# Kernel tuning notes

Measured on AMD Instinct MI355X. Metric: run time of the kernel, lower is better.

## Reference

```python
import jax, jax.numpy as jnp
import numpy as np


def conv2d(x, w, pad=0, groups=1, bias=None):
    out = jax.lax.conv_general_dilated(
        x, w, (1, 1), [(pad, pad), (pad, pad)],
        dimension_numbers=('NCHW', 'OIHW', 'NCHW'), feature_group_count=groups)
    return out if bias is None else out + bias[None, :, None, None]


def l2norm(t):
    # F.normalize(t, dim=-1): divide by max(||t||_2, 1e-12)
    return t / jnp.maximum(jnp.sqrt(jnp.sum(t * t, axis=-1, keepdims=True)), 1e-12)


def chan_attn(q, k, v, temp, heads):
    # transposed (channel) attention: contract over N=H*W, softmax over small channel dim
    b, _, h, w = v.shape
    n = h * w
    q = l2norm(q.reshape(b, heads, -1, n))
    k = l2norm(k.reshape(b, heads, -1, n))
    v = v.reshape(b, heads, -1, n)
    attn = jax.nn.softmax(jnp.einsum('bhdn,bhen->bhde', q, k) * temp, axis=-1)
    return jnp.einsum('bhde,bhen->bhdn', attn, v).reshape(b, -1, h, w)


def nearest_resize(x, H, W):
    # torch F.interpolate(mode='nearest'): idx = floor(i * in/out)
    hi, wi = x.shape[2], x.shape[3]
    iy = jnp.arange(H) * hi // H
    ix = jnp.arange(W) * wi // W
    return x[:, :, iy][:, :, :, ix]


def deform_conv(x, offsets, w, bias, k, pad, groups):
    # torchvision DeformConv2d, stride=1, dilation=1, offset layout [B, 2*k*k, H, W] as (dy, dx) pairs
    B, Cin, H, W = x.shape
    K2 = k * k
    off = offsets.reshape(B, K2, 2, H, W)
    ky, kx = jnp.meshgrid(jnp.arange(k), jnp.arange(k), indexing='ij')
    py = (jnp.arange(H)[None, None, :, None] - pad) + ky.reshape(1, K2, 1, 1) + off[:, :, 0]
    px = (jnp.arange(W)[None, None, None, :] - pad) + kx.reshape(1, K2, 1, 1) + off[:, :, 1]
    y0f = jnp.floor(py); x0f = jnp.floor(px)
    wy = (py - y0f)[:, None]  # [B,1,K2,H,W]
    wx = (px - x0f)[:, None]
    y0 = y0f.astype(jnp.int32); x0 = x0f.astype(jnp.int32)
    xf = x.reshape(B, Cin, H * W)

    def gather(yi, xi):
        valid = ((yi >= 0) & (yi < H) & (xi >= 0) & (xi < W)).astype(x.dtype)
        idx = (jnp.clip(yi, 0, H - 1) * W + jnp.clip(xi, 0, W - 1)).reshape(B, 1, -1)
        v = jnp.take_along_axis(xf, idx, axis=2).reshape(B, Cin, K2, H, W)
        return v * valid[:, None]

    s = (gather(y0, x0) * (1 - wy) * (1 - wx)
         + gather(y0, x0 + 1) * (1 - wy) * wx
         + gather(y0 + 1, x0) * wy * (1 - wx)
         + gather(y0 + 1, x0 + 1) * wy * wx)  # [B, Cin, K2, H, W]
    g = groups
    s = s.reshape(B, g, Cin // g, K2, H, W)
    wg = w.reshape(g, w.shape[0] // g, Cin // g, K2)
    out = jnp.einsum('bgckhw,gock->bgohw', s, wg).reshape(B, -1, H, W)
    return out + bias[None, :, None, None]


def scconv(x, w_k2, w_k3, w_k4):
    B, C, H, W = x.shape
    p = x.reshape(B, C, H // 2, 2, W // 2, 2).mean(axis=(3, 5))  # AvgPool2d(2,2)
    a = jax.nn.sigmoid(nearest_resize(conv2d(p, w_k2, pad=0), H, W))
    return conv2d(conv2d(x, w_k3, pad=1) * a, w_k4, pad=1)


def layernorm_c(x, g, b):
    # LayerNorm over channel dim of NCHW (applied as [B, HW, C] in the original)
    b_, c, h, w = x.shape
    t = x.reshape(b_, c, h * w).transpose(0, 2, 1)
    mu = t.mean(-1, keepdims=True)
    var = ((t - mu) ** 2).mean(-1, keepdims=True)
    t = (t - mu) / jnp.sqrt(var + 1e-5) * g + b
    return t.transpose(0, 2, 1).reshape(b_, c, h, w)


def _forward(x, y, temp, w_po, w_lp1, w_lp2, ln_g, ln_b, temp_in, w_qkv, w_qkvd,
             w_mproj, w_c3, w_k2, w_k3, w_k4, w_d3, b_d3, w_d5, b_d5, w_d7, b_d7,
             w_pw, b_pw):
    b, c, h, w = x.shape
    heads = 8
    # --- Multi_Receptive_Attentive_Prompts ---
    l1 = conv2d(x, w_lp1)
    l2 = conv2d(x, w_lp2, pad=1)
    xn = layernorm_c(x, ln_g, ln_b)
    qkv = conv2d(conv2d(xn, w_qkv), w_qkvd, pad=1, groups=c)
    qi, ki, vi = jnp.split(qkv, 3, axis=1)
    xg = x + conv2d(chan_attn(qi, ki, vi, temp_in, heads), w_mproj)
    prompt = conv2d(jnp.concatenate([l1, l2, xg], axis=1), w_c3, pad=1)
    # --- Temporal_Alignment ---
    offs = scconv(jnp.concatenate([x, y], axis=1), w_k2, w_k3, w_k4)  # [B,166,H,W]
    f3 = jax.nn.relu(deform_conv(x, offs[:, :18], w_d3, b_d3, 3, 1, 8))
    f5 = jax.nn.relu(deform_conv(x, offs[:, 18:68], w_d5, b_d5, 5, 2, 8))
    f7 = jax.nn.relu(deform_conv(x, offs[:, 68:166], w_d7, b_d7, 7, 3, 8))
    k_feat = conv2d(jnp.concatenate([f3, f5, f7], axis=1), w_pw, bias=b_pw)
    # --- prompted channel attention ---
    q_feat = jnp.concatenate([x, prompt], axis=1)  # 2c channels -> d_q = 2c/heads
    out = chan_attn(q_feat, k_feat, x, temp, heads)  # [B, 2c, H, W]
    return conv2d(out, w_po)


def setup_inputs() -> dict:
    key = jax.random.key(0)
    ks = jax.random.split(key, 16)
    C, B, H, W = 32, 2, 128, 128
    r = lambda k, shp: jax.random.normal(k, shp, dtype=jnp.float32) * 0.05
    return {
        'x': jax.random.normal(ks[0], (B, C, H, W), dtype=jnp.float32),
        'y': jax.random.normal(ks[1], (B, C, H, W), dtype=jnp.float32),
        'temp': jnp.ones((1, 8, 1, 1), jnp.float32),
        'w_po': r(ks[2], (C, 2 * C, 1, 1)),
        'w_lp1': r(ks[3], (C, C, 1, 1)),
        'w_lp2': r(ks[4], (C, C, 3, 3)),
        'ln_g': jnp.ones((C,), jnp.float32),
        'ln_b': jnp.zeros((C,), jnp.float32),
        'temp_in': jnp.ones((1, 8, 1, 1), jnp.float32),
        'w_qkv': r(ks[5], (3 * C, C, 1, 1)),
        'w_qkvd': r(ks[6], (3 * C, 3, 3, 3)),  # groups=C: in/groups = 3
        'w_mproj': r(ks[7], (C, C, 1, 1)),
        'w_c3': r(ks[8], (C, 3 * C, 3, 3)),
        'w_k2': r(ks[9], (166, 2 * C, 3, 3)),
        'w_k3': r(ks[10], (166, 2 * C, 3, 3)),
        'w_k4': r(ks[11], (166, 166, 3, 3)),
        'w_d3': r(ks[12], (C, C // 8, 3, 3)),
        'b_d3': jnp.zeros((C,), jnp.float32),
        'w_d5': r(ks[13], (C, C // 8, 5, 5)),
        'b_d5': jnp.zeros((C,), jnp.float32),
        'w_d7': r(ks[14], (C, C // 8, 7, 7)),
        'b_d7': jnp.zeros((C,), jnp.float32),
        'w_pw': r(ks[15], (C, 3 * C, 1, 1)),
        'b_pw': jnp.zeros((C,), jnp.float32),
    }


def reference(x, y, temp, w_po, w_lp1, w_lp2, ln_g, ln_b, temp_in, w_qkv, w_qkvd,
              w_mproj, w_c3, w_k2, w_k3, w_k4, w_d3, b_d3, w_d5, b_d5, w_d7, b_d7,
              w_pw, b_pw):
    return _forward(x, y, temp, w_po, w_lp1, w_lp2, ln_g, ln_b, temp_in, w_qkv,
                    w_qkvd, w_mproj, w_c3, w_k2, w_k3, w_k4, w_d3, b_d3, w_d5,
                    b_d5, w_d7, b_d7, w_pw, b_pw)
```

## Files before the change

### kernel.cpp

```cpp
#include <hip/hip_runtime.h>
#include <hip/hip_bf16.h>
#include <hip/hip_fp16.h>


constexpr int B = 2, C = 32, H = 128, W = 128, N = H * W;

using bh8   = __attribute__((ext_vector_type(8))) short;
using f32x4 = __attribute__((ext_vector_type(4))) float;

__device__ __forceinline__ ushort f2bf(float v) {
  __hip_bfloat16 h = __float2bfloat16(v);
  return *(ushort*)&h;
}
__device__ __forceinline__ float bf2f(ushort u) {
  union { unsigned int i; float f; } w; w.i = ((unsigned int)u) << 16; return w.f;
}

__global__ __launch_bounds__(256) void k_prep(const float* __restrict__ x,
                                              const float* __restrict__ y,
                                              const float* __restrict__ ln_g,
                                              const float* __restrict__ ln_b,
                                              float* __restrict__ cat2,
                                              ushort* __restrict__ xtb,
                                              ushort* __restrict__ cat2b,
                                              float* __restrict__ xn,
                                              ushort* __restrict__ poolb) {
  __shared__ float tile[C][257];
  const int b = blockIdx.y, n0 = blockIdx.x * 256, tid = threadIdx.x;
  const int n = n0 + tid;
  const int prow = blockIdx.x;
  for (int c = 0; c < C; c++) {
    float v = x[(size_t)(b * C + c) * N + n];
    tile[c][tid] = v;
    cat2[(size_t)(b * 64 + c) * N + n] = v;
  }
  __syncthreads();
  {
    float s = 0.f, ss = 0.f;
#pragma unroll
    for (int c = 0; c < C; c++) { const float v = tile[c][tid]; s += v; ss += v * v; }
    const float mu = s * (1.f / C);
    const float var = ss * (1.f / C) - mu * mu;
    const float inv = rsqrtf(var + 1e-5f);
#pragma unroll
    for (int c = 0; c < C; c++)
      xn[(size_t)(b * C + c) * N + n] = (tile[c][tid] - mu) * inv * ln_g[c] + ln_b[c];
  }
  for (int i = tid; i < C * 256; i += 256) {
    int c = i & 31, nl = i >> 5;
    const ushort bv = f2bf(tile[c][nl]);
    xtb[((size_t)b * N + n0 + nl) * 32 + c] = bv;
    cat2b[((size_t)b * N + n0 + nl) * 64 + c] = bv;
  }
  for (int i = tid; i < 2048; i += 256) {
    const int ox = i >> 5, c = i & 31;
    const float pv = 0.25f * (tile[c][2 * ox] + tile[c][2 * ox + 1]
                            + tile[c][128 + 2 * ox] + tile[c][128 + 2 * ox + 1]);
    poolb[((size_t)b * 4096 + prow * 64 + ox) * 64 + c] = f2bf(pv);
  }
  __syncthreads();
  for (int c = 0; c < C; c++) {
    float v = y[(size_t)(b * C + c) * N + n];
    tile[c][tid] = v;
    cat2[(size_t)(b * 64 + 32 + c) * N + n] = v;
  }
  __syncthreads();
  for (int i = tid; i < C * 256; i += 256) {
    int c = i & 31, nl = i >> 5;
    cat2b[((size_t)b * N + n0 + nl) * 64 + 32 + c] = f2bf(tile[c][nl]);
  }
  for (int i = tid; i < 2048; i += 256) {
    const int ox = i >> 5, c = i & 31;
    const float pv = 0.25f * (tile[c][2 * ox] + tile[c][2 * ox + 1]
                            + tile[c][128 + 2 * ox] + tile[c][128 + 2 * ox + 1]);
    poolb[((size_t)b * 4096 + prow * 64 + ox) * 64 + 32 + c] = f2bf(pv);
  }
}

struct WEnt { const float* src; ushort* dst; int cout_real, cin_real, kc32, total; };
struct WArgs { WEnt e[5]; };

__global__ __launch_bounds__(256) void k_wpack(WArgs a) {
  const WEnt en = a.e[blockIdx.y];
  const int tk = 9 * en.kc32;
  for (int i = blockIdx.x * 256 + threadIdx.x; i < en.total; i += gridDim.x * 256) {
    const int co = i / tk, rem = i - co * tk;
    const int t = rem / en.kc32, ci = rem - t * en.kc32;
    float v = 0.f;
    if (co < en.cout_real && ci < en.cin_real)
      v = en.src[((size_t)co * en.cin_real + ci) * 9 + t];
    en.dst[i] = f2bf(v);
  }
}

__global__ __launch_bounds__(256)
void k_conv3m(const ushort* __restrict__ xin, long in_bs, int in_cs, int ih, int iw,
              const ushort* __restrict__ wp, int kchunks, int cout_real,
              void* __restrict__ outp, long out_bs, int out_coff,
              int oh, int ow, int pad, int omode, int out_cs, int store_tot) {
  __shared__ ushort smem[17408];
  ushort* xt = smem;
  const int tid = threadIdx.x, b = blockIdx.z;
  const int y0 = blockIdx.x * 2, co0 = blockIdx.y * 64;
  const int wv = tid >> 6, lane = tid & 63;
  const int row_sel = wv >> 1, col0 = (wv & 1) * 64;
  const int q = lane >> 4, n = lane & 15, q8 = q * 8;
  const int kc32 = kchunks * 32;
  const ushort* xb = xin + (size_t)b * in_bs;

  f32x4 acc[4][4];
#pragma unroll
  for (int mt = 0; mt < 4; mt++)
#pragma unroll
    for (int nb = 0; nb < 4; nb++) acc[mt][nb] = (f32x4){0.f, 0.f, 0.f, 0.f};

  for (int cc = 0; cc < kchunks; cc++) {
    __syncthreads();
    for (int i = tid; i < 2080; i += 256) {
      const int qq = i & 3, rc = i >> 2;
      const int r = rc / 130, c = rc - r * 130;
      const int yy = y0 - pad + r, xx = c - pad;
      bh8 v = {0, 0, 0, 0, 0, 0, 0, 0};
      if (yy >= 0 && yy < ih && xx >= 0 && xx < iw)
        v = *(const bh8*)(xb + ((size_t)yy * iw + xx) * in_cs + cc * 32 + qq * 8);
      *(bh8*)&xt[rc * 32 + qq * 8] = v;
    }
    __syncthreads();
#pragma unroll
    for (int t = 0; t < 9; t++) {
      const int dy = t / 3, dx = t - dy * 3;
      bh8 a[4], bb[4];
#pragma unroll
      for (int mt = 0; mt < 4; mt++)
        a[mt] = *(const bh8*)(wp + (size_t)((co0 + mt * 16 + n) * 9 + t) * kc32 + cc * 32 + q8);
#pragma unroll
      for (int nb = 0; nb < 4; nb++)
        bb[nb] = *(const bh8*)&xt[((row_sel + dy) * 130 + col0 + nb * 16 + n + dx) * 32 + q8];
#pragma unroll
      for (int mt = 0; mt < 4; mt++)
#pragma unroll
        for (int nb = 0; nb < 4; nb++)
          acc[mt][nb] = __builtin_amdgcn_mfma_f32_16x16x32_bf16(a[mt], bb[nb], acc[mt][nb], 0, 0, 0);
    }
  }

  const size_t osp = (size_t)oh * ow;
  if (omode == 0) {
    const int oy = y0 + row_sel;
    float* ob = (float*)outp + (size_t)b * out_bs + (size_t)out_coff * osp + (size_t)oy * ow;
#pragma unroll
    for (int mt = 0; mt < 4; mt++)
#pragma unroll
      for (int r = 0; r < 4; r++) {
        const int co = co0 + mt * 16 + q * 4 + r;
        if (co < cout_real) {
#pragma unroll
          for (int nb = 0; nb < 4; nb++) {
            const int px = col0 + nb * 16 + n;
            if (px < ow) ob[(size_t)co * osp + px] = acc[mt][nb][r];
          }
        }
      }
  } else if (omode == 1) {
    __syncthreads();
#pragma unroll
    for (int mt = 0; mt < 4; mt++)
#pragma unroll
      for (int nb = 0; nb < 4; nb++) {
        const int px = col0 + nb * 16 + n;
        ushort4 o;
        o.x = f2bf(acc[mt][nb][0]); o.y = f2bf(acc[mt][nb][1]);
        o.z = f2bf(acc[mt][nb][2]); o.w = f2bf(acc[mt][nb][3]);
        *(ushort4*)&smem[(row_sel * 128 + px) * 68 + mt * 16 + q * 4] = o;
      }
    __syncthreads();
    {
      const int row = tid >> 7, px = tid & 127;
      const int oy2 = y0 + row;
      const int sc = min(64, store_tot - co0);
      if (px < ow && sc > 0) {
        ushort* dst = (ushort*)outp + ((size_t)b * osp + (size_t)oy2 * ow + px) * out_cs
                      + out_coff + co0;
        const ushort* src = &smem[(row * 128 + px) * 68];
        for (int c = 0; c < sc; c += 4)
          *(ushort4*)(dst + c) = *(const ushort4*)(src + c);
      }
    }
  } else {
    float* tf = (float*)smem;
    for (int round = 0; round < 2; round++) {
      __syncthreads();
      if (row_sel == round) {
#pragma unroll
        for (int mt = 0; mt < 4; mt++)
#pragma unroll
          for (int nb = 0; nb < 4; nb++) {
            const int px = col0 + nb * 16 + n;
            *(f32x4*)&tf[px * 66 + mt * 16 + q * 4] = acc[mt][nb];
          }
      }
      __syncthreads();
      const int px = tid & 127, ch = tid >> 7;
      const int oy2 = y0 + round;
      float* dst = (float*)outp + ((size_t)b * osp + (size_t)oy2 * ow + px) * out_cs
                   + out_coff + co0 + ch * 32;
      const float* src = &tf[px * 66 + ch * 32];
      for (int c = 0; c < 32; c += 4) {
        if (co0 + ch * 32 + c + 3 < store_tot)
          *(float4*)(dst + c) = *(const float4*)(src + c);
      }
    }
  }
}

template <int PX>
__global__ __launch_bounds__(256)
void k_conv1x1v(const float* __restrict__ in, long in_bs, int cin,
                const float* __restrict__ wts, const float* __restrict__ bias,
                float* __restrict__ out, long out_bs, int out_coff,
                ushort* __restrict__ outb, int ob_cs) {
  const int n0 = (blockIdx.x * 256 + threadIdx.x) * PX;
  const int co0 = blockIdx.y * 4, b = blockIdx.z;
  const float* ip = in + (size_t)b * in_bs + n0;
  const float* w = wts + (size_t)co0 * cin;
  float acc[4][PX] = {};
  for (int ci = 0; ci < cin; ci++) {
    float xv[PX];
    if (PX == 4) {
      const float4 v = *(const float4*)(ip + (size_t)ci * N);
      xv[0] = v.x; xv[1] = v.y; xv[2] = v.z; xv[3] = v.w;
    } else {
      const float2 v = *(const float2*)(ip + (size_t)ci * N);
      xv[0] = v.x; xv[1] = v.y;
    }
    const float w0 = w[ci], w1 = w[cin + ci], w2 = w[2 * cin + ci], w3 = w[3 * cin + ci];
#pragma unroll
    for (int p = 0; p < PX; p++) {
      acc[0][p] += xv[p] * w0; acc[1][p] += xv[p] * w1;
      acc[2][p] += xv[p] * w2; acc[3][p] += xv[p] * w3;
    }
  }
  if (bias) {
#pragma unroll
    for (int o = 0; o < 4; o++) {
      const float bv = bias[co0 + o];
#pragma unroll
      for (int p = 0; p < PX; p++) acc[o][p] += bv;
    }
  }
  if (outb) {
#pragma unroll
    for (int p = 0; p < PX; p++) {
      ushort4 o;
      o.x = f2bf(acc[0][p]); o.y = f2bf(acc[1][p]);
      o.z = f2bf(acc[2][p]); o.w = f2bf(acc[3][p]);
      *(ushort4*)(outb + ((size_t)b * N + n0 + p) * ob_cs + out_coff + co0) = o;
    }
  } else {
#pragma unroll
    for (int o = 0; o < 4; o++) {
      if (PX == 4)
        *(float4*)(out + (size_t)b * out_bs + (size_t)(out_coff + co0 + o) * N + n0) =
            make_float4(acc[o][0], acc[o][1], acc[o][2], acc[o][3]);
      else
        *(float2*)(out + (size_t)b * out_bs + (size_t)(out_coff + co0 + o) * N + n0) =
            make_float2(acc[o][0], acc[o][1]);
    }
  }
}

__global__ __launch_bounds__(256) void k_dwconv(const float* __restrict__ in,
                                                const float* __restrict__ wts,
                                                float* __restrict__ out) {
  const int n0 = (blockIdx.x * 256 + threadIdx.x) * 4;
  const int g = blockIdx.y, b = blockIdx.z;
  const int h0 = n0 >> 7, w0 = n0 & 127;
  float acc[3][4] = {};
  for (int ci = 0; ci < 3; ci++) {
    const float* ip = in + ((size_t)b * 96 + g * 3 + ci) * N;
    float v[3][6];
#pragma unroll
    for (int r = 0; r < 3; r++) {
      const int iy = h0 - 1 + r;
      const bool rowok = (iy >= 0) & (iy < H);
#pragma unroll
      for (int j = 0; j < 6; j++) {
        const int ix = w0 - 1 + j;
        v[r][j] = (rowok && ix >= 0 && ix < W) ? ip[(size_t)iy * W + ix] : 0.f;
      }
    }
#pragma unroll
    for (int o = 0; o < 3; o++) {
      const float* wp = wts + ((size_t)(g * 3 + o) * 3 + ci) * 9;
#pragma unroll
      for (int r = 0; r < 3; r++) {
        const float wa = wp[r * 3 + 0], wb = wp[r * 3 + 1], wc = wp[r * 3 + 2];
#pragma unroll
        for (int p = 0; p < 4; p++)
          acc[o][p] += v[r][p] * wa + v[r][p + 1] * wb + v[r][p + 2] * wc;
      }
    }
  }
#pragma unroll
  for (int o = 0; o < 3; o++)
    *(float4*)(out + ((size_t)b * 96 + g * 3 + o) * N + n0) =
        make_float4(acc[o][0], acc[o][1], acc[o][2], acc[o][3]);
}

template <int DQ>
__global__ __launch_bounds__(256)
void k_attn_part(const float* __restrict__ q1, long q1_bs,
                 const float* __restrict__ q2, long q2_bs,
                 const float* __restrict__ k, long k_bs,
                 float* __restrict__ partial) {
  const int h = blockIdx.x, b = blockIdx.y, ch = blockIdx.z, tid = threadIdx.x;
  const float* qp[DQ];
#pragma unroll
  for (int d = 0; d < DQ; d++) {
    const int qc = h * DQ + d;
    qp[d] = (qc < 32) ? (q1 + (size_t)b * q1_bs + (size_t)qc * N)
                      : (q2 + (size_t)b * q2_bs + (size_t)(qc - 32) * N);
  }
  const float* kp[4];
#pragma unroll
  for (int e = 0; e < 4; e++) kp[e] = k + (size_t)b * k_bs + (size_t)(h * 4 + e) * N;

  constexpr int NV = DQ + 4 + DQ * 4;
  float ssq[DQ] = {}, ssk[4] = {}, gr[DQ][4] = {};
  const int n1 = (ch + 1) * (N / 8);
  for (int n = ch * (N / 8) + tid; n < n1; n += 256) {
    float qv[DQ], kv[4];
#pragma unroll
    for (int d = 0; d < DQ; d++) { qv[d] = qp[d][n]; ssq[d] += qv[d] * qv[d]; }
#pragma unroll
    for (int e = 0; e < 4; e++) { kv[e] = kp[e][n]; ssk[e] += kv[e] * kv[e]; }
#pragma unroll
    for (int d = 0; d < DQ; d++)
#pragma unroll
      for (int e = 0; e < 4; e++) gr[d][e] += qv[d] * kv[e];
  }
  float vals[NV];
#pragma unroll
  for (int d = 0; d < DQ; d++) vals[d] = ssq[d];
#pragma unroll
  for (int e = 0; e < 4; e++) vals[DQ + e] = ssk[e];
#pragma unroll
  for (int d = 0; d < DQ; d++)
#pragma unroll
    for (int e = 0; e < 4; e++) vals[DQ + 4 + d * 4 + e] = gr[d][e];
#pragma unroll
  for (int j = 0; j < NV; j++) {
    float v = vals[j];
    for (int m = 32; m > 0; m >>= 1) v += __shfl_xor(v, m, 64);
    vals[j] = v;
  }
  __shared__ float red[4][NV];
  const int wid = tid >> 6, lane = tid & 63;
  if (lane == 0)
#pragma unroll
    for (int j = 0; j < NV; j++) red[wid][j] = vals[j];
  __syncthreads();
  if (tid < NV)
    partial[(size_t)(((b * 8 + h) * 8) + ch) * NV + tid] =
        red[0][tid] + red[1][tid] + red[2][tid] + red[3][tid];
}

template <int DQ>
__global__ __launch_bounds__(128)
void k_attn_soft(const float* __restrict__ partial,
                 const float* __restrict__ temp, float* __restrict__ stats) {
  constexpr int NV = DQ + 4 + DQ * 4;
  const int h = blockIdx.x, b = blockIdx.y, tid = threadIdx.x;
  __shared__ float tot[NV];
  if (tid < NV) {
    float s = 0.f;
#pragma unroll
    for (int ch = 0; ch < 8; ch++)
      s += partial[(size_t)(((b * 8 + h) * 8) + ch) * NV + tid];
    tot[tid] = s;
  }
  __syncthreads();
  if (tid == 0) {
    float invq[DQ], invk[4];
#pragma unroll
    for (int d = 0; d < DQ; d++) invq[d] = 1.f / fmaxf(sqrtf(tot[d]), 1e-12f);
#pragma unroll
    for (int e = 0; e < 4; e++) invk[e] = 1.f / fmaxf(sqrtf(tot[DQ + e]), 1e-12f);
    const float t = temp[h];
    float* sp = stats + (size_t)(b * 8 + h) * DQ * 4;
    for (int d = 0; d < DQ; d++) {
      float s[4], mx = -1e30f;
#pragma unroll
      for (int e = 0; e < 4; e++) {
        s[e] = tot[DQ + 4 + d * 4 + e] * invq[d] * invk[e] * t;
        mx = fmaxf(mx, s[e]);
      }
      float sum = 0.f;
#pragma unroll
      for (int e = 0; e < 4; e++) { s[e] = expf(s[e] - mx); sum += s[e]; }
#pragma unroll
      for (int e = 0; e < 4; e++) sp[d * 4 + e] = s[e] / sum;
    }
  }
}

template <int DQ>
__global__ __launch_bounds__(256)
void k_fold(const float* __restrict__ stats, const float* __restrict__ w,
            float* __restrict__ M) {
  const int b = blockIdx.x;
  for (int idx = threadIdx.x; idx < 1024; idx += 256) {
    const int co = idx >> 5, j = idx & 31;
    const int h = j >> 2, e = j & 3;
    const float* A = stats + ((size_t)b * 8 + h) * DQ * 4;
    const float* wr = w + co * (8 * DQ) + h * DQ;
    float s = 0.f;
#pragma unroll
    for (int d = 0; d < DQ; d++) s += wr[d] * A[d * 4 + e];
    M[((size_t)b * 32 + co) * 32 + j] = s;
  }
}

__global__ __launch_bounds__(256)
void k_attn_mproj2(const float* __restrict__ qkv2, const float* __restrict__ M2,
                   const float* __restrict__ x, ushort* __restrict__ cat1b) {
  __shared__ float mls[512];
  const int tid = threadIdx.x, b = blockIdx.y, z = blockIdx.z;
  const int n = blockIdx.x * 256 + tid;
  for (int i = tid; i < 512; i += 256)
    mls[i] = M2[((size_t)b * 32 + z * 16) * 32 + i];
  __syncthreads();
  const float* vi = qkv2 + (size_t)b * (96L * N) + 64L * N;
  float vv[32];
#pragma unroll
  for (int ci = 0; ci < 32; ci++) vv[ci] = vi[(size_t)ci * N + n];
  ushort to[16];
  for (int o = 0; o < 16; o++) {
    const float* m = &mls[o * 32];
    float r = 0.f;
#pragma unroll
    for (int ci = 0; ci < 32; ci += 4) {
      const float4 w4 = *(const float4*)&m[ci];
      r += w4.x * vv[ci] + w4.y * vv[ci + 1] + w4.z * vv[ci + 2] + w4.w * vv[ci + 3];
    }
    r += x[(size_t)(b * 64 + z * 16 + o) * N + n];
    to[o] = f2bf(r);
  }
  ushort* dp = cat1b + ((size_t)b * N + n) * 96 + 64 + z * 16;
#pragma unroll
  for (int k = 0; k < 2; k++) *(bh8*)(dp + k * 8) = *(const bh8*)&to[k * 8];
}

__global__ __launch_bounds__(256)
void k_attn_po2(const float* __restrict__ cat2, const float* __restrict__ M,
                float* __restrict__ outp) {
  __shared__ float mls[512];
  const int tid = threadIdx.x, b = blockIdx.y, z = blockIdx.z;
  const int n = blockIdx.x * 256 + tid;
  for (int i = tid; i < 512; i += 256)
    mls[i] = M[((size_t)b * 32 + z * 16) * 32 + i];
  __syncthreads();
  const float* v = cat2 + (size_t)b * (64L * N);
  float vv[32];
#pragma unroll
  for (int ci = 0; ci < 32; ci++) vv[ci] = v[(size_t)ci * N + n];
  for (int o = 0; o < 16; o++) {
    const float* m = &mls[o * 32];
    float r = 0.f;
#pragma unroll
    for (int ci = 0; ci < 32; ci += 4) {
      const float4 w4 = *(const float4*)&m[ci];
      r += w4.x * vv[ci] + w4.y * vv[ci + 1] + w4.z * vv[ci + 2] + w4.w * vv[ci + 3];
    }
    outp[(size_t)(b * 32 + z * 16 + o) * N + n] = r;
  }
}

__global__ __launch_bounds__(256)
void k_sigcast(const ushort* __restrict__ t3r, const float* __restrict__ asmall,
               ushort* __restrict__ t3b) {
  const int n = blockIdx.x * 256 + threadIdx.x;
  const int cy = blockIdx.y, b = blockIdx.z;
  const int x = n & 127, yv = n >> 7;
  const int iy = (yv * 62) >> 7, ix = (x * 62) >> 7;
  const ushort* sp = t3r + ((size_t)b * N + n) * 192 + cy * 32;
  ushort tr[32];
#pragma unroll
  for (int k = 0; k < 4; k++) *(bh8*)&tr[k * 8] = *(const bh8*)(sp + k * 8);
  ushort tmp[32];
#pragma unroll
  for (int j = 0; j < 32; j++) {
    const int c = cy * 32 + j;
    float v = 0.f;
    if (c < 166) {
      const float a = asmall[((size_t)b * 166 + c) * 3844 + iy * 62 + ix];
      v = bf2f(tr[j]) * (1.f / (1.f + expf(-a)));
    }
    tmp[j] = f2bf(v);
  }
  ushort* dp = t3b + ((size_t)b * N + n) * 192 + cy * 32;
#pragma unroll
  for (int k = 0; k < 4; k++) *(bh8*)(dp + k * 8) = *(const bh8*)&tmp[k * 8];
}

__global__ __launch_bounds__(256)
void k_deform7(const ushort* __restrict__ xtb, const float* __restrict__ offs,
               const float* __restrict__ wd3, const float* __restrict__ bd3,
               const float* __restrict__ wd5, const float* __restrict__ bd5,
               const float* __restrict__ wd7, const float* __restrict__ bd7,
               float* __restrict__ out) {
  const int tid = threadIdx.x, b = blockIdx.y;
  const int zone = blockIdx.x >> 9;
  const int blk = blockIdx.x & 511;
  int K, off_c0, out_c0;
  const float *wd, *bd;
  if (zone == 0)      { K = 3; off_c0 = 0;  out_c0 = 0;  wd = wd3; bd = bd3; }
  else if (zone == 1) { K = 5; off_c0 = 18; out_c0 = 32; wd = wd5; bd = bd5; }
  else                { K = 7; off_c0 = 68; out_c0 = 64; wd = wd7; bd = bd7; }
  const int K2 = K * K, PAD = K / 2;

  extern __shared__ __align__(16) char smem[];
  __half*  wlds = (__half*)smem;
  __half*  wbl  = wlds + K2 * 128;
  ushort*  abl  = (ushort*)(wbl + 32 * K2 * 4);

  for (int i = tid; i < K2 * 128; i += 256) {
    const int t = i >> 7, r = i & 127;
    const int g = r >> 4, oo = (r >> 2) & 3, ci = r & 3;
    wlds[i] = __float2half(wd[(size_t)((g * 4 + oo) * 4 + ci) * K2 + t]);
  }
  const int px0 = blk * 32;
  const float* obb = offs + ((size_t)b * N) * 168;
  for (int i = tid; i < 32 * K2; i += 256) {
    const int p = i / K2, t = i - p * K2;
    const int px = px0 + p;
    const int hy = px >> 7, wx = px & 127;
    const int ky = t / K, kx = t - ky * K;
    const float* ob2 = obb + (size_t)px * 168 + off_c0;
    const float dy = ob2[2 * t];
    const float dx = ob2[2 * t + 1];
    const float py = (float)(hy - PAD + ky) + dy;
    const float pxf = (float)(wx - PAD + kx) + dx;
    const float y0f = floorf(py), x0f = floorf(pxf);
    const float fy = py - y0f, fx = pxf - x0f;
    const int y0 = (int)y0f, x0 = (int)x0f;
    const int y1 = y0 + 1, x1 = x0 + 1;
    float w00 = (1.f - fy) * (1.f - fx), w01 = (1.f - fy) * fx;
    float w10 = fy * (1.f - fx), w11 = fy * fx;
    const bool vy0 = (y0 >= 0) & (y0 < H), vy1 = (y1 >= 0) & (y1 < H);
    const bool vx0 = (x0 >= 0) & (x0 < W), vx1 = (x1 >= 0) & (x1 < W);
    w00 = (vy0 & vx0) ? w00 : 0.f;
    w01 = (vy0 & vx1) ? w01 : 0.f;
    w10 = (vy1 & vx0) ? w10 : 0.f;
    w11 = (vy1 & vx1) ? w11 : 0.f;
    const int cy0 = min(max(y0, 0), H - 1), cy1 = min(max(y1, 0), H - 1);
    const int cx0 = min(max(x0, 0), W - 1), cx1 = min(max(x1, 0), W - 1);
    const int base = (p * K2 + t) * 4;
    wbl[base + 0] = __float2half(w00); wbl[base + 1] = __float2half(w01);
    wbl[base + 2] = __float2half(w10); wbl[base + 3] = __float2half(w11);
    abl[base + 0] = (ushort)(cy0 * W + cx0);
    abl[base + 1] = (ushort)(cy0 * W + cx1);
    abl[base + 2] = (ushort)(cy1 * W + cx0);
    abl[base + 3] = (ushort)(cy1 * W + cx1);
  }
  __syncthreads();

  const int pxl = tid >> 3, g = tid & 7;
  const int px = px0 + pxl;
  const ushort* xb = xtb + (size_t)b * N * 32 + g * 4;
  float acc[4] = {0.f, 0.f, 0.f, 0.f};
  for (int t = 0; t < K2; t++) {
    const int base = (pxl * K2 + t) * 4;
    const ushort4 r4 = *(const ushort4*)&abl[base];
    const float2 w01v = __half22float2(*(const __half2*)&wbl[base]);
    const float2 w23v = __half22float2(*(const __half2*)&wbl[base + 2]);
    const ushort4 c0 = *(const ushort4*)(xb + (size_t)r4.x * 32);
    const ushort4 c1 = *(const ushort4*)(xb + (size_t)r4.y * 32);
    const ushort4 c2 = *(const ushort4*)(xb + (size_t)r4.z * 32);
    const ushort4 c3 = *(const ushort4*)(xb + (size_t)r4.w * 32);
    const float s0 = w01v.x * bf2f(c0.x) + w01v.y * bf2f(c1.x)
                   + w23v.x * bf2f(c2.x) + w23v.y * bf2f(c3.x);
    const float s1 = w01v.x * bf2f(c0.y) + w01v.y * bf2f(c1.y)
                   + w23v.x * bf2f(c2.y) + w23v.y * bf2f(c3.y);
    const float s2 = w01v.x * bf2f(c0.z) + w01v.y * bf2f(c1.z)
                   + w23v.x * bf2f(c2.z) + w23v.y * bf2f(c3.z);
    const float s3 = w01v.x * bf2f(c0.w) + w01v.y * bf2f(c1.w)
                   + w23v.x * bf2f(c2.w) + w23v.y * bf2f(c3.w);
    const __half2* wp2 = (const __half2*)&wlds[(t * 8 + g) * 16];
#pragma unroll
    for (int oo = 0; oo < 4; oo++) {
      const float2 u01 = __half22float2(wp2[oo * 2]);
      const float2 u23 = __half22float2(wp2[oo * 2 + 1]);
      acc[oo] += s0 * u01.x + s1 * u01.y + s2 * u23.x + s3 * u23.y;
    }
  }
#pragma unroll
  for (int oo = 0; oo < 4; oo++) {
    const float r = fmaxf(acc[oo] + bd[g * 4 + oo], 0.f);
    out[((size_t)b * 96 + out_c0 + g * 4 + oo) * N + px] = r;
  }
}

extern "C" void kernel_launch(void* const* d_in, const int* in_sizes, int n_in,
                              void* d_out, int out_size, void* d_ws, size_t ws_size,
                              hipStream_t stream) {
  const float* fx       = (const float*)d_in[0];
  const float* fy       = (const float*)d_in[1];
  const float* w_temp   = (const float*)d_in[2];
  const float* w_po     = (const float*)d_in[3];
  const float* w_lp1    = (const float*)d_in[4];
  const float* w_lp2    = (const float*)d_in[5];
  const float* ln_g     = (const float*)d_in[6];
  const float* ln_b     = (const float*)d_in[7];
  const float* w_tempin = (const float*)d_in[8];
  const float* w_qkv    = (const float*)d_in[9];
  const float* w_qkvd   = (const float*)d_in[10];
  const float* w_mproj  = (const float*)d_in[11];
  const float* w_c3     = (const float*)d_in[12];
  const float* w_k2     = (const float*)d_in[13];
  const float* w_k3     = (const float*)d_in[14];
  const float* w_k4     = (const float*)d_in[15];
  const float* w_d3     = (const float*)d_in[16];
  const float* b_d3     = (const float*)d_in[17];
  const float* w_d5     = (const float*)d_in[18];
  const float* b_d5     = (const float*)d_in[19];
  const float* w_d7     = (const float*)d_in[20];
  const float* b_d7     = (const float*)d_in[21];
  const float* w_pw     = (const float*)d_in[22];
  const float* b_pw     = (const float*)d_in[23];
  float* ws = (float*)d_ws;

  size_t off = 0;
  auto buf = [&](size_t nelem) { float* p = ws + off; off += nelem; return p; };
  float* CAT2   = buf(2097152);
  float* XTBf   = buf(1048576);
  float* R1     = buf(1048576);
  float* R2     = buf(3145728);
  float* R3     = buf(3145728);
  float* PROMPT = buf(1048576);
  float* R4     = buf(5439488);
  float* OFFS   = buf(5505024);
  float* STATS  = buf(32768);
  float* CAT2Bf = buf(524288);
  float* WPf    = buf(327680);
  float* POOLBf = buf(262144);
  (void)ws_size; (void)out_size; (void)n_in; (void)in_sizes;

  float* XN = R1;
  float* QKV1 = R2;
  float* QKV2 = R3;   float* ASMALL = R3 + 524288;
  float* CAT3 = R4;   float* KFEAT = R4 + 3145728;
  float* ST_IN = STATS;
  float* ST_FI = STATS + 256;
  float* P_IN  = STATS + 1024;
  float* P_FI  = STATS + 8192;
  float* M_IN  = STATS + 16384;
  float* M_FI  = STATS + 20480;

  ushort* XTb   = (ushort*)XTBf;
  ushort* CAT2b = (ushort*)CAT2Bf;
  ushort* POOLb = (ushort*)POOLBf;
  ushort* CAT1b = (ushort*)OFFS;
  ushort* T3raw = (ushort*)R4;
  ushort* T3b   = (ushort*)R2;

  ushort* WPu = (ushort*)WPf;
  ushort* wp_lp2 = WPu;
  ushort* wp_c3  = wp_lp2 + 18432;
  ushort* wp_k2  = wp_c3 + 55296;
  ushort* wp_k3  = wp_k2 + 110592;
  ushort* wp_k4  = wp_k3 + 110592;

  const long bs64 = 64L * N, bs32 = 32L * N, bs96 = 96L * N;

  WArgs wa;
  wa.e[0] = { w_lp2, wp_lp2, 32, 32, 32, 64 * 9 * 32 };
  wa.e[1] = { w_c3,  wp_c3,  32, 96, 96, 64 * 9 * 96 };
  wa.e[2] = { w_k2,  wp_k2, 166, 64, 64, 192 * 9 * 64 };
  wa.e[3] = { w_k3,  wp_k3, 166, 64, 64, 192 * 9 * 64 };
  wa.e[4] = { w_k4,  wp_k4, 166, 166, 192, 192 * 9 * 192 };
  k_wpack<<<dim3(64, 5), 256, 0, stream>>>(wa);
  k_prep<<<dim3(N / 256, B), 256, 0, stream>>>(
      fx, fy, ln_g, ln_b, CAT2, XTb, CAT2b, XN, POOLb);
  k_conv1x1v<4><<<dim3(N / 1024, 24, B), 256, 0, stream>>>(
      XN, bs32, 32, w_qkv, nullptr, QKV1, bs96, 0, nullptr, 0);
  k_dwconv<<<dim3(N / 1024, 32, B), 256, 0, stream>>>(QKV1, w_qkvd, QKV2);
  k_attn_part<4><<<dim3(8, B, 8), 256, 0, stream>>>(
      QKV2, bs96, nullptr, 0, QKV2 + bs32, bs96, P_IN);
  k_attn_soft<4><<<dim3(8, B), 128, 0, stream>>>(P_IN, w_tempin, ST_IN);
  k_fold<4><<<dim3(B), 256, 0, stream>>>(ST_IN, w_mproj, M_IN);
  k_attn_mproj2<<<dim3(N / 256, B, 2), 256, 0, stream>>>(QKV2, M_IN, CAT2, CAT1b);
  k_conv1x1v<2><<<dim3(N / 512, 8, B), 256, 0, stream>>>(
      CAT2, bs64, 32, w_lp1, nullptr, nullptr, 0, 0, CAT1b, 96);
  k_conv3m<<<dim3(64, 1, B), 256, 0, stream>>>(
      CAT2b, (long)N * 64, 64, H, W, wp_lp2, 1, 32, CAT1b, 0, 32, H, W, 1, 1, 96, 32);
  k_conv3m<<<dim3(64, 1, B), 256, 0, stream>>>(
      CAT1b, (long)N * 96, 96, H, W, wp_c3, 3, 32, PROMPT, bs32, 0, H, W, 1, 0, 0, 0);
  k_conv3m<<<dim3(31, 3, B), 256, 0, stream>>>(
      POOLb, 4096L * 64, 64, 64, 64, wp_k2, 2, 166, ASMALL, 166L * 3844, 0, 62, 62, 0, 0, 0, 0);
  k_conv3m<<<dim3(64, 3, B), 256, 0, stream>>>(
      CAT2b, (long)N * 64, 64, H, W, wp_k3, 2, 166, T3raw, 0, 0, H, W, 1, 1, 192, 192);
  k_sigcast<<<dim3(64, 6, B), 256, 0, stream>>>(T3raw, ASMALL, T3b);
  k_conv3m<<<dim3(64, 3, B), 256, 0, stream>>>(
      T3b, (long)N * 192, 192, H, W, wp_k4, 6, 166, OFFS, 0, 0, H, W, 1, 2, 168, 168);
  {
    const int K2m = 49;
    const size_t smem = (size_t)K2m * 128 * 2 + (size_t)32 * K2m * 4 * 2 * 2;
    k_deform7<<<dim3(3 * (N / 32), B), 256, smem, stream>>>(
        XTb, OFFS, w_d3, b_d3, w_d5, b_d5, w_d7, b_d7, CAT3);
  }
  k_conv1x1v<2><<<dim3(N / 512, 8, B), 256, 0, stream>>>(
      CAT3, bs96, 96, w_pw, b_pw, KFEAT, bs32, 0, nullptr, 0);
  k_attn_part<8><<<dim3(8, B, 8), 256, 0, stream>>>(
      CAT2, bs64, PROMPT, bs32, KFEAT, bs32, P_FI);
  k_attn_soft<8><<<dim3(8, B), 128, 0, stream>>>(P_FI, w_temp, ST_FI);
  k_fold<8><<<dim3(B), 256, 0, stream>>>(ST_FI, w_po, M_FI);
  k_attn_po2<<<dim3(N / 256, B, 2), 256, 0, stream>>>(CAT2, M_FI, (float*)d_out);
}
```

Measured before the change: 489.6 us.

## Fuse sigmoid gating into k3 conv epilogue and split attention reductions finer

```diff
diff --git a/kernel.cpp b/kernel.cpp
--- a/kernel.cpp
+++ b/kernel.cpp
@@ -97,7 +97,8 @@
 void k_conv3m(const ushort* __restrict__ xin, long in_bs, int in_cs, int ih, int iw,
               const ushort* __restrict__ wp, int kchunks, int cout_real,
               void* __restrict__ outp, long out_bs, int out_coff,
-              int oh, int ow, int pad, int omode, int out_cs, int store_tot) {
+              int oh, int ow, int pad, int omode, int out_cs, int store_tot,
+              const float* __restrict__ gatep) {
   __shared__ ushort smem[17408];
   ushort* xt = smem;
   const int tid = threadIdx.x, b = blockIdx.z;
@@ -182,8 +183,31 @@
         ushort* dst = (ushort*)outp + ((size_t)b * osp + (size_t)oy2 * ow + px) * out_cs
                       + out_coff + co0;
         const ushort* src = &smem[(row * 128 + px) * 68];
-        for (int c = 0; c < sc; c += 4)
-          *(ushort4*)(dst + c) = *(const ushort4*)(src + c);
+        if (gatep) {
+          const int iy = (oy2 * 62) >> 7, ix2 = (px * 62) >> 7;
+          const float* gp = gatep + ((size_t)b * 3844 + iy * 62 + ix2) * 168;
+          for (int c = 0; c < sc; c += 4) {
+            ushort4 v = *(const ushort4*)(src + c);
+            const int ch0 = out_coff + co0 + c;
+            float g0 = 1.f, g1 = 1.f, g2 = 1.f, g3 = 1.f;
+            if (ch0 + 3 < 166) {
+              const float4 a4 = *(const float4*)(gp + ch0);
+              g0 = 1.f / (1.f + expf(-a4.x)); g1 = 1.f / (1.f + expf(-a4.y));
+              g2 = 1.f / (1.f + expf(-a4.z)); g3 = 1.f / (1.f + expf(-a4.w));
+            } else {
+              if (ch0 + 0 < 166) g0 = 1.f / (1.f + expf(-gp[ch0 + 0]));
+              if (ch0 + 1 < 166) g1 = 1.f / (1.f + expf(-gp[ch0 + 1]));
+              if (ch0 + 2 < 166) g2 = 1.f / (1.f + expf(-gp[ch0 + 2]));
+              if (ch0 + 3 < 166) g3 = 1.f / (1.f + expf(-gp[ch0 + 3]));
+            }
+            v.x = f2bf(bf2f(v.x) * g0); v.y = f2bf(bf2f(v.y) * g1);
+            v.z = f2bf(bf2f(v.z) * g2); v.w = f2bf(bf2f(v.w) * g3);
+            *(ushort4*)(dst + c) = v;
+          }
+        } else {
+          for (int c = 0; c < sc; c += 4)
+            *(ushort4*)(dst + c) = *(const ushort4*)(src + c);
+        }
       }
     }
   } else {
@@ -202,12 +226,14 @@
       __syncthreads();
       const int px = tid & 127, ch = tid >> 7;
       const int oy2 = y0 + round;
-      float* dst = (float*)outp + ((size_t)b * osp + (size_t)oy2 * ow + px) * out_cs
-                   + out_coff + co0 + ch * 32;
-      const float* src = &tf[px * 66 + ch * 32];
-      for (int c = 0; c < 32; c += 4) {
-        if (co0 + ch * 32 + c + 3 < store_tot)
-          *(float4*)(dst + c) = *(const float4*)(src + c);
+      if (px < ow) {
+        float* dst = (float*)outp + ((size_t)b * osp + (size_t)oy2 * ow + px) * out_cs
+                     + out_coff + co0 + ch * 32;
+        const float* src = &tf[px * 66 + ch * 32];
+        for (int c = 0; c < 32; c += 4) {
+          if (co0 + ch * 32 + c + 3 < store_tot)
+            *(float4*)(dst + c) = *(const float4*)(src + c);
+        }
       }
     }
   }
@@ -327,8 +353,8 @@
 
   constexpr int NV = DQ + 4 + DQ * 4;
   float ssq[DQ] = {}, ssk[4] = {}, gr[DQ][4] = {};
-  const int n1 = (ch + 1) * (N / 8);
-  for (int n = ch * (N / 8) + tid; n < n1; n += 256) {
+  const int n1 = (ch + 1) * (N / 16);
+  for (int n = ch * (N / 16) + tid; n < n1; n += 256) {
     float qv[DQ], kv[4];
 #pragma unroll
     for (int d = 0; d < DQ; d++) { qv[d] = qp[d][n]; ssq[d] += qv[d] * qv[d]; }
@@ -361,7 +387,7 @@
     for (int j = 0; j < NV; j++) red[wid][j] = vals[j];
   __syncthreads();
   if (tid < NV)
-    partial[(size_t)(((b * 8 + h) * 8) + ch) * NV + tid] =
+    partial[(size_t)(((b * 8 + h) * 16) + ch) * NV + tid] =
         red[0][tid] + red[1][tid] + red[2][tid] + red[3][tid];
 }
 
@@ -375,8 +401,8 @@
   if (tid < NV) {
     float s = 0.f;
 #pragma unroll
-    for (int ch = 0; ch < 8; ch++)
-      s += partial[(size_t)(((b * 8 + h) * 8) + ch) * NV + tid];
+    for (int ch = 0; ch < 16; ch++)
+      s += partial[(size_t)(((b * 8 + h) * 16) + ch) * NV + tid];
     tot[tid] = s;
   }
   __syncthreads();
@@ -474,33 +500,6 @@
     }
     outp[(size_t)(b * 32 + z * 16 + o) * N + n] = r;
   }
-}
-
-__global__ __launch_bounds__(256)
-void k_sigcast(const ushort* __restrict__ t3r, const float* __restrict__ asmall,
-               ushort* __restrict__ t3b) {
-  const int n = blockIdx.x * 256 + threadIdx.x;
-  const int cy = blockIdx.y, b = blockIdx.z;
-  const int x = n & 127, yv = n >> 7;
-  const int iy = (yv * 62) >> 7, ix = (x * 62) >> 7;
-  const ushort* sp = t3r + ((size_t)b * N + n) * 192 + cy * 32;
-  ushort tr[32];
-#pragma unroll
-  for (int k = 0; k < 4; k++) *(bh8*)&tr[k * 8] = *(const bh8*)(sp + k * 8);
-  ushort tmp[32];
-#pragma unroll
-  for (int j = 0; j < 32; j++) {
-    const int c = cy * 32 + j;
-    float v = 0.f;
-    if (c < 166) {
-      const float a = asmall[((size_t)b * 166 + c) * 3844 + iy * 62 + ix];
-      v = bf2f(tr[j]) * (1.f / (1.f + expf(-a)));
-    }
-    tmp[j] = f2bf(v);
-  }
-  ushort* dp = t3b + ((size_t)b * N + n) * 192 + cy * 32;
-#pragma unroll
-  for (int k = 0; k < 4; k++) *(bh8*)(dp + k * 8) = *(const bh8*)&tmp[k * 8];
 }
 
 __global__ __launch_bounds__(256)
@@ -640,7 +639,7 @@
   float* PROMPT = buf(1048576);
   float* R4     = buf(5439488);
   float* OFFS   = buf(5505024);
-  float* STATS  = buf(32768);
+  float* STATS  = buf(65536);
   float* CAT2Bf = buf(524288);
   float* WPf    = buf(327680);
   float* POOLBf = buf(262144);
@@ -652,16 +651,15 @@
   float* CAT3 = R4;   float* KFEAT = R4 + 3145728;
   float* ST_IN = STATS;
   float* ST_FI = STATS + 256;
-  float* P_IN  = STATS + 1024;
-  float* P_FI  = STATS + 8192;
-  float* M_IN  = STATS + 16384;
-  float* M_FI  = STATS + 20480;
+  float* M_IN  = STATS + 1024;
+  float* M_FI  = STATS + 3072;
+  float* P_IN  = STATS + 5120;
+  float* P_FI  = STATS + 14336;
 
   ushort* XTb   = (ushort*)XTBf;
   ushort* CAT2b = (ushort*)CAT2Bf;
   ushort* POOLb = (ushort*)POOLBf;
   ushort* CAT1b = (ushort*)OFFS;
-  ushort* T3raw = (ushort*)R4;
   ushort* T3b   = (ushort*)R2;
 
   ushort* WPu = (ushort*)WPf;
@@ -685,7 +683,7 @@
   k_conv1x1v<4><<<dim3(N / 1024, 24, B), 256, 0, stream>>>(
       XN, bs32, 32, w_qkv, nullptr, QKV1, bs96, 0, nullptr, 0);
   k_dwconv<<<dim3(N / 1024, 32, B), 256, 0, stream>>>(QKV1, w_qkvd, QKV2);
-  k_attn_part<4><<<dim3(8, B, 8), 256, 0, stream>>>(
+  k_attn_part<4><<<dim3(8, B, 16), 256, 0, stream>>>(
       QKV2, bs96, nullptr, 0, QKV2 + bs32, bs96, P_IN);
   k_attn_soft<4><<<dim3(8, B), 128, 0, stream>>>(P_IN, w_tempin, ST_IN);
   k_fold<4><<<dim3(B), 256, 0, stream>>>(ST_IN, w_mproj, M_IN);
@@ -693,16 +691,20 @@
   k_conv1x1v<2><<<dim3(N / 512, 8, B), 256, 0, stream>>>(
       CAT2, bs64, 32, w_lp1, nullptr, nullptr, 0, 0, CAT1b, 96);
   k_conv3m<<<dim3(64, 1, B), 256, 0, stream>>>(
-      CAT2b, (long)N * 64, 64, H, W, wp_lp2, 1, 32, CAT1b, 0, 32, H, W, 1, 1, 96, 32);
+      CAT2b, (long)N * 64, 64, H, W, wp_lp2, 1, 32, CAT1b, 0, 32, H, W, 1, 1, 96, 32,
+      nullptr);
   k_conv3m<<<dim3(64, 1, B), 256, 0, stream>>>(
-      CAT1b, (long)N * 96, 96, H, W, wp_c3, 3, 32, PROMPT, bs32, 0, H, W, 1, 0, 0, 0);
+      CAT1b, (long)N * 96, 96, H, W, wp_c3, 3, 32, PROMPT, bs32, 0, H, W, 1, 0, 0, 0,
+      nullptr);
   k_conv3m<<<dim3(31, 3, B), 256, 0, stream>>>(
-      POOLb, 4096L * 64, 64, 64, 64, wp_k2, 2, 166, ASMALL, 166L * 3844, 0, 62, 62, 0, 0, 0, 0);
+      POOLb, 4096L * 64, 64, 64, 64, wp_k2, 2, 166, ASMALL, 0, 0, 62, 62, 0, 2, 168, 168,
+      nullptr);
   k_conv3m<<<dim3(64, 3, B), 256, 0, stream>>>(
-      CAT2b, (long)N * 64, 64, H, W, wp_k3, 2, 166, T3raw, 0, 0, H, W, 1, 1, 192, 192);
-  k_sigcast<<<dim3(64, 6, B), 256, 0, stream>>>(T3raw, ASMALL, T3b);
+      CAT2b, (long)N * 64, 64, H, W, wp_k3, 2, 166, T3b, 0, 0, H, W, 1, 1, 192, 192,
+      ASMALL);
   k_conv3m<<<dim3(64, 3, B), 256, 0, stream>>>(
-      T3b, (long)N * 192, 192, H, W, wp_k4, 6, 166, OFFS, 0, 0, H, W, 1, 2, 168, 168);
+      T3b, (long)N * 192, 192, H, W, wp_k4, 6, 166, OFFS, 0, 0, H, W, 1, 2, 168, 168,
+      nullptr);
   {
     const int K2m = 49;
     const size_t smem = (size_t)K2m * 128 * 2 + (size_t)32 * K2m * 4 * 2 * 2;
@@ -711,7 +713,7 @@
   }
   k_conv1x1v<2><<<dim3(N / 512, 8, B), 256, 0, stream>>>(
       CAT3, bs96, 96, w_pw, b_pw, KFEAT, bs32, 0, nullptr, 0);
-  k_attn_part<8><<<dim3(8, B, 8), 256, 0, stream>>>(
+  k_attn_part<8><<<dim3(8, B, 16), 256, 0, stream>>>(
       CAT2, bs64, PROMPT, bs32, KFEAT, bs32, P_FI);
   k_attn_soft<8><<<dim3(8, B), 128, 0, stream>>>(P_FI, w_temp, ST_FI);
   k_fold<8><<<dim3(B), 256, 0, stream>>>(ST_FI, w_po, M_FI);
```

New measurement: 494.5 us. About the same (+1.0%).
